# Kernel tuning notes

Hardware: AMD Instinct MI355X
Metric: run time of the kernel (lower is better)

## Reference

```python
import jax, jax.numpy as jnp
import numpy as np

E = 1024
H = 16
D = E // H  # projection_dim = 64


def setup_inputs() -> dict:
    key = jax.random.key(0)
    ks = jax.random.split(key, 9)
    s = 1.0 / np.sqrt(E)
    return {
        "inputs": jax.random.normal(ks[0], (2, 2048, E), dtype=jnp.float32),
        "Wq": jax.random.uniform(ks[1], (E, E), jnp.float32, -s, s),
        "bq": jax.random.uniform(ks[2], (E,), jnp.float32, -s, s),
        "Wk": jax.random.uniform(ks[3], (E, E), jnp.float32, -s, s),
        "bk": jax.random.uniform(ks[4], (E,), jnp.float32, -s, s),
        "Wv": jax.random.uniform(ks[5], (E, E), jnp.float32, -s, s),
        "bv": jax.random.uniform(ks[6], (E,), jnp.float32, -s, s),
        "Wo": jax.random.uniform(ks[7], (E, E), jnp.float32, -s, s),
        "bo": jax.random.uniform(ks[8], (E,), jnp.float32, -s, s),
    }


def reference(inputs, Wq, bq, Wk, bk, Wv, bv, Wo, bo):
    B, S, _ = inputs.shape
    # Linear layers use y = x @ W.T + b (torch convention); weights here stored as [E,E]
    q = inputs @ Wq.T + bq
    k = inputs @ Wk.T + bk
    v = inputs @ Wv.T + bv
    # separate heads: [B,S,E] -> [B,H,S,D]
    q = q.reshape(B, S, H, D).transpose(0, 2, 1, 3)
    k = k.reshape(B, S, H, D).transpose(0, 2, 1, 3)
    v = v.reshape(B, S, H, D).transpose(0, 2, 1, 3)
    scale = 1.0 / jnp.sqrt(jnp.float32(D))
    scores = jnp.einsum('bhqd,bhkd->bhqk', q, k) * scale  # [B,H,S,S]
    weights = jax.nn.softmax(scores, axis=-1)
    attn = jnp.einsum('bhqk,bhkd->bhqd', weights, v)  # [B,H,S,D]
    concat = attn.transpose(0, 2, 1, 3).reshape(B, S, E)
    # dropout is identity in eval mode
    return concat @ Wo.T + bo
```

## Files before the change

kernel.cpp:

```cpp
#include <hip/hip_runtime.h>
#include <hip/hip_bf16.h>
#include <stdint.h>

#define E_ 1024
#define H_ 16
#define D_ 64
#define B_ 2
#define S_ 2048
#define M_ 4096

typedef __bf16 bf16_t;
typedef __bf16 bf16x8 __attribute__((ext_vector_type(8)));
typedef __bf16 bf16x4 __attribute__((ext_vector_type(4)));
typedef __bf16 bf16x2 __attribute__((ext_vector_type(2)));
typedef float  f32x4  __attribute__((ext_vector_type(4)));
typedef float  f32x16 __attribute__((ext_vector_type(16)));
typedef unsigned int u32x2 __attribute__((ext_vector_type(2)));
typedef unsigned int u32x4 __attribute__((ext_vector_type(4)));

__global__ __launch_bounds__(256) void cvt_f32_to_bf16(const float* __restrict__ src,
                                                       bf16_t* __restrict__ dst, int n4) {
  int i = blockIdx.x * blockDim.x + threadIdx.x;
  if (i < n4) {
    float4 v = reinterpret_cast<const float4*>(src)[i];
    bf16x4 o;
    o[0] = (bf16_t)v.x; o[1] = (bf16_t)v.y; o[2] = (bf16_t)v.z; o[3] = (bf16_t)v.w;
    reinterpret_cast<bf16x4*>(dst)[i] = o;
  }
}

__global__ __launch_bounds__(256) void cvt_weights(
    const float* __restrict__ w0, const float* __restrict__ w1,
    const float* __restrict__ w2, const float* __restrict__ w3,
    bf16_t* __restrict__ d0, bf16_t* __restrict__ d1,
    bf16_t* __restrict__ d2, bf16_t* __restrict__ d3) {
  const int z = blockIdx.y;
  const float* src = (z == 0) ? w0 : (z == 1) ? w1 : (z == 2) ? w2 : w3;
  bf16_t* dst = (z == 0) ? d0 : (z == 1) ? d1 : (z == 2) ? d2 : d3;
  int i = blockIdx.x * blockDim.x + threadIdx.x;
  float4 v = reinterpret_cast<const float4*>(src)[i];
  bf16x4 o;
  o[0] = (bf16_t)v.x; o[1] = (bf16_t)v.y; o[2] = (bf16_t)v.z; o[3] = (bf16_t)v.w;
  reinterpret_cast<bf16x4*>(dst)[i] = o;
}

static __device__ __forceinline__ void gl_lds16(const bf16_t* g, bf16_t* l) {
  __builtin_amdgcn_global_load_lds((__attribute__((address_space(1))) void*)g,
                                   (__attribute__((address_space(3))) void*)l,
                                   16, 0, 0);
}

__global__ __launch_bounds__(512) void qkv_gemm256(
    const bf16_t* __restrict__ xbf, const bf16_t* __restrict__ Wqkv,
    const float* __restrict__ bq, const float* __restrict__ bk, const float* __restrict__ bv,
    bf16_t* __restrict__ Qo, bf16_t* __restrict__ Ko, bf16_t* __restrict__ Vt) {
  __shared__ alignas(16) bf16_t lA[4][256 * 32];
  __shared__ alignas(16) bf16_t lB[4][256 * 32];
  const int tid = threadIdx.x, lane = tid & 63, wave = tid >> 6;
  const int wr = wave >> 2, wc = wave & 3;
  const int lrow = lane & 15, lgrp = lane >> 4;
  const int m0 = blockIdx.x << 8, n0 = blockIdx.y << 8;

  const int srow = tid >> 2;
  const int scolg = (tid & 3) ^ ((srow >> 1) & 3);
  const char* sA0 = (const char*)xbf  + (size_t)(m0 + srow) * 2048 + scolg * 16;
  const char* sB0 = (const char*)Wqkv + (size_t)(n0 + srow) * 2048 + scolg * 16;

  auto STAGE = [&](int T) {
    const int buf = T & 3;
    const char* a = sA0 + T * 64;
    const char* b = sB0 + T * 64;
    gl_lds16((const bf16_t*)a,                        &lA[buf][tid * 8]);
    gl_lds16((const bf16_t*)(a + (size_t)128 * 2048), &lA[buf][4096 + tid * 8]);
    gl_lds16((const bf16_t*)b,                        &lB[buf][tid * 8]);
    gl_lds16((const bf16_t*)(b + (size_t)128 * 2048), &lB[buf][4096 + tid * 8]);
  };

  f32x4 acc[8][4];
  const f32x4 zero = {0.f, 0.f, 0.f, 0.f};
#pragma unroll
  for (int i = 0; i < 8; i++)
#pragma unroll
    for (int j = 0; j < 4; j++) acc[i][j] = zero;

  const int rswz = (lgrp ^ ((lrow >> 1) & 3)) * 16;
  const int rdA = (wr * 128 + lrow) * 64 + rswz;
  const int rdB = (wc * 64 + lrow) * 64 + rswz;

  auto KTILE = [&](int T) {
    const int buf = T & 3;
    const char* kA = (const char*)&lA[buf][0] + rdA;
    const char* kB = (const char*)&lB[buf][0] + rdB;
    bf16x8 fA[8], fB[4];
#pragma unroll
    for (int i = 0; i < 8; i++) fA[i] = *reinterpret_cast<const bf16x8*>(kA + i * 1024);
#pragma unroll
    for (int j = 0; j < 4; j++) fB[j] = *reinterpret_cast<const bf16x8*>(kB + j * 1024);
    __builtin_amdgcn_s_setprio(1);
#pragma unroll
    for (int i = 0; i < 8; i++)
#pragma unroll
      for (int j = 0; j < 4; j++)
        acc[i][j] = __builtin_amdgcn_mfma_f32_16x16x32_bf16(fA[i], fB[j], acc[i][j], 0, 0, 0);
    __builtin_amdgcn_s_setprio(0);
  };

  STAGE(0); STAGE(1); STAGE(2);
  asm volatile("s_waitcnt vmcnt(8)" ::: "memory");
  __builtin_amdgcn_s_barrier();
  __builtin_amdgcn_sched_barrier(0);

  for (int T = 0; T < 29; ++T) {
    STAGE(T + 3);
    KTILE(T);
    asm volatile("s_waitcnt vmcnt(8)" ::: "memory");
    __builtin_amdgcn_s_barrier();
    __builtin_amdgcn_sched_barrier(0);
  }
  KTILE(29);
  asm volatile("s_waitcnt vmcnt(4)" ::: "memory");
  __builtin_amdgcn_s_barrier();
  __builtin_amdgcn_sched_barrier(0);
  KTILE(30);
  asm volatile("s_waitcnt vmcnt(0)" ::: "memory");
  __builtin_amdgcn_s_barrier();
  __builtin_amdgcn_sched_barrier(0);
  KTILE(31);

  const int z = n0 >> 10;
  const float* bias = (z == 0) ? bq : ((z == 1) ? bk : bv);
  const int nloc_base = (n0 & 1023) + wc * 64;
  if (z == 2) {
#pragma unroll
    for (int i = 0; i < 8; i++) {
      const int mb = m0 + wr * 128 + i * 16 + lgrp * 4;
      const int b_ = mb >> 11, s = mb & (S_ - 1);
#pragma unroll
      for (int j = 0; j < 4; j++) {
        const int nl = nloc_base + j * 16 + lrow;
        const float bn = bias[nl];
        const int h = nl >> 6, d = nl & 63;
        bf16x4 v;
#pragma unroll
        for (int r = 0; r < 4; r++) v[r] = (bf16_t)(acc[i][j][r] + bn);
        *reinterpret_cast<bf16x4*>(Vt + ((size_t)((b_ * H_ + h) * D_ + d)) * S_ + s) = v;
      }
    }
  } else {
    bf16_t* O = z ? Ko : Qo;
    const float scale = (z == 0) ? 0.18033688011112042f : 1.0f;
#pragma unroll
    for (int i = 0; i < 8; i++) {
      const int mb = m0 + wr * 128 + i * 16 + lgrp * 4;
      const int b_ = mb >> 11, s = mb & (S_ - 1);
#pragma unroll
      for (int j = 0; j < 4; j++) {
        const int nl = nloc_base + j * 16 + lrow;
        const float bn = bias[nl];
        const int h = nl >> 6, d = nl & 63;
#pragma unroll
        for (int r = 0; r < 4; r++)
          O[((size_t)((b_ * H_ + h) * S_) + (s + r)) * D_ + d] = (bf16_t)((acc[i][j][r] + bn) * scale);
      }
    }
  }
}

template <int SWAP>
static __device__ __forceinline__ void gemm128_mainloop(
    const bf16_t* __restrict__ Ag, const bf16_t* __restrict__ Bg,
    bf16_t* ldsA0, bf16_t* ldsA1, bf16_t* ldsB0, bf16_t* ldsB1,
    int m0, int n0, f32x4 acc[4][4]) {
  const int tid  = threadIdx.x;
  const int lane = tid & 63, wave = tid >> 6;
  const int lrow = lane & 15, lgrp = lane >> 4;
  const int wr = (wave >> 1) * 64, wc = (wave & 1) * 64;
  const int skol = (lane & 3) * 8;
  const int c0 = wave * 2;
  const int rowA = c0 * 16 + (lane >> 2);
  const f32x4 zero = {0.f, 0.f, 0.f, 0.f};
#pragma unroll
  for (int i = 0; i < 4; i++)
#pragma unroll
    for (int j = 0; j < 4; j++) acc[i][j] = zero;

  gl_lds16(Ag + (size_t)(m0 + rowA) * E_ + skol,      ldsA0 + c0 * 512);
  gl_lds16(Ag + (size_t)(m0 + rowA + 16) * E_ + skol, ldsA0 + (c0 + 1) * 512);
  gl_lds16(Bg + (size_t)(n0 + rowA) * E_ + skol,      ldsB0 + c0 * 512);
  gl_lds16(Bg + (size_t)(n0 + rowA + 16) * E_ + skol, ldsB0 + (c0 + 1) * 512);
  __syncthreads();

  for (int kt = 0; kt < E_ / 32; ++kt) {
    bf16_t* sA = (kt & 1) ? ldsA1 : ldsA0;
    bf16_t* sB = (kt & 1) ? ldsB1 : ldsB0;
    if (kt + 1 < E_ / 32) {
      bf16_t* dA = (kt & 1) ? ldsA0 : ldsA1;
      bf16_t* dB = (kt & 1) ? ldsB0 : ldsB1;
      const int k0 = (kt + 1) * 32;
      gl_lds16(Ag + (size_t)(m0 + rowA) * E_ + k0 + skol,      dA + c0 * 512);
      gl_lds16(Ag + (size_t)(m0 + rowA + 16) * E_ + k0 + skol, dA + (c0 + 1) * 512);
      gl_lds16(Bg + (size_t)(n0 + rowA) * E_ + k0 + skol,      dB + c0 * 512);
      gl_lds16(Bg + (size_t)(n0 + rowA + 16) * E_ + k0 + skol, dB + (c0 + 1) * 512);
    }
    bf16x8 fA[4], fB[4];
#pragma unroll
    for (int i = 0; i < 4; i++)
      fA[i] = *reinterpret_cast<const bf16x8*>(sA + (wr + i * 16 + lrow) * 32 + lgrp * 8);
#pragma unroll
    for (int j = 0; j < 4; j++)
      fB[j] = *reinterpret_cast<const bf16x8*>(sB + (wc + j * 16 + lrow) * 32 + lgrp * 8);
#pragma unroll
    for (int i = 0; i < 4; i++)
#pragma unroll
      for (int j = 0; j < 4; j++)
        acc[i][j] = SWAP
          ? __builtin_amdgcn_mfma_f32_16x16x32_bf16(fB[j], fA[i], acc[i][j], 0, 0, 0)
          : __builtin_amdgcn_mfma_f32_16x16x32_bf16(fA[i], fB[j], acc[i][j], 0, 0, 0);
    __syncthreads();
  }
}

__global__ __launch_bounds__(256) void out_gemm(
    const bf16_t* __restrict__ Cbf, const bf16_t* __restrict__ Wob,
    const float* __restrict__ bo, float* __restrict__ out) {
  __shared__ alignas(16) bf16_t ldsA[2][128 * 32];
  __shared__ alignas(16) bf16_t ldsB[2][128 * 32];
  const int m0 = blockIdx.x * 128, n0 = blockIdx.y * 128;
  f32x4 acc[4][4];
  gemm128_mainloop<1>(Cbf, Wob, ldsA[0], ldsA[1], ldsB[0], ldsB[1], m0, n0, acc);

  const int lane = threadIdx.x & 63, wave = threadIdx.x >> 6;
  const int lrow = lane & 15, lgrp = lane >> 4;
  const int wr = (wave >> 1) * 64, wc = (wave & 1) * 64;
#pragma unroll
  for (int i = 0; i < 4; i++) {
    const int m = m0 + wr + i * 16 + lrow;
#pragma unroll
    for (int j = 0; j < 4; j++) {
      const int nb = n0 + wc + j * 16 + lgrp * 4;
      const f32x4 b4 = *reinterpret_cast<const f32x4*>(bo + nb);
      f32x4 v = acc[i][j] + b4;
      *reinterpret_cast<f32x4*>(out + (size_t)m * E_ + nb) = v;
    }
  }
}


static __device__ __forceinline__ unsigned pack2(float a, float b) {
  bf16x2 t; t[0] = (bf16_t)a; t[1] = (bf16_t)b;
  return __builtin_bit_cast(unsigned, t);
}

static __device__ __forceinline__ bf16x8 mkfrag(unsigned a0, unsigned a1,
                                                unsigned a2, unsigned a3) {
  u32x2 s02 = __builtin_amdgcn_permlane32_swap(a0, a2, false, false);
  u32x2 s13 = __builtin_amdgcn_permlane32_swap(a1, a3, false, false);
  u32x4 t; t[0] = s02[0]; t[1] = s13[0]; t[2] = s02[1]; t[3] = s13[1];
  return *reinterpret_cast<bf16x8*>(&t);
}

__global__ __launch_bounds__(512) void attn_kernel(
    const bf16_t* __restrict__ Qg, const bf16_t* __restrict__ Kg,
    const bf16_t* __restrict__ Vtg, bf16_t* __restrict__ Og) {
  __shared__ alignas(16) bf16_t Kl[2][2][64 * 64];
  __shared__ alignas(16) bf16_t Vl[2][2][64 * 64];
  const int f = blockIdx.x;
  const int bh = (f & 7) * 4 + (f >> 7);
  const int q0 = ((f >> 3) & 15) * 128;
  const int tid = threadIdx.x, lane = tid & 63, wave = tid >> 6;
  const int qsub = wave & 3, kvg = wave >> 2;
  const int ql = lane & 31, hi = lane >> 5;
  const bf16_t* Qb = Qg + (size_t)bh * S_ * D_;
  const bf16_t* Kb = Kg + (size_t)bh * S_ * D_;
  const bf16_t* Vb = Vtg + (size_t)bh * D_ * S_;

  const int q = q0 + qsub * 32 + ql;
  bf16x8 qf[4];
#pragma unroll
  for (int ds = 0; ds < 4; ds++)
    qf[ds] = *reinterpret_cast<const bf16x8*>(Qb + (size_t)q * D_ + ds * 16 + hi * 8);

  f32x16 o0, o1;
#pragma unroll
  for (int r = 0; r < 16; r++) { o0[r] = 0.f; o1[r] = 0.f; }
  float li = 0.f;

  const int srow_lo = lane >> 3;
  const int sunit = lane & 7;

#pragma unroll
  for (int p = 0; p < 2; p++) {
    int c = p * 4 + qsub;
    int row = c * 8 + srow_lo;
    int u = sunit ^ (row & 7);
    gl_lds16(Kb + (size_t)(kvg * 64 + row) * D_ + u * 8, &Kl[kvg][0][c * 512]);
    gl_lds16(Vb + (size_t)row * S_ + kvg * 64 + u * 8, &Vl[kvg][0][c * 512]);
  }
  __syncthreads();

  for (int it = 0; it < S_ / 128; ++it) {
    const int cur = it & 1;
    if (it + 1 < S_ / 128) {
      const int kvn = (kvg + (it + 1) * 2) * 64;
#pragma unroll
      for (int p = 0; p < 2; p++) {
        int c = p * 4 + qsub;
        int row = c * 8 + srow_lo;
        int u = sunit ^ (row & 7);
        gl_lds16(Kb + (size_t)(kvn + row) * D_ + u * 8, &Kl[kvg][cur ^ 1][c * 512]);
        gl_lds16(Vb + (size_t)row * S_ + kvn + u * 8, &Vl[kvg][cur ^ 1][c * 512]);
      }
    }
    const char* kbuf = reinterpret_cast<const char*>(&Kl[kvg][cur][0]);
    const char* vbuf = reinterpret_cast<const char*>(&Vl[kvg][cur][0]);

    f32x16 pa0, pa1;
#pragma unroll
    for (int r = 0; r < 16; r++) { pa0[r] = 0.f; pa1[r] = 0.f; }
    __builtin_amdgcn_s_setprio(1);
#pragma unroll
    for (int ds = 0; ds < 4; ds++) {
      {
        const int krow = ql;
        const int u = (ds * 2 + hi) ^ (krow & 7);
        bf16x8 kf = *reinterpret_cast<const bf16x8*>(kbuf + krow * 128 + u * 16);
        pa0 = __builtin_amdgcn_mfma_f32_32x32x16_bf16(kf, qf[ds], pa0, 0, 0, 0);
      }
      {
        const int krow = 32 + ql;
        const int u = (ds * 2 + hi) ^ (krow & 7);
        bf16x8 kf = *reinterpret_cast<const bf16x8*>(kbuf + krow * 128 + u * 16);
        pa1 = __builtin_amdgcn_mfma_f32_32x32x16_bf16(kf, qf[ds], pa1, 0, 0, 0);
      }
    }
    __builtin_amdgcn_s_setprio(0);

    float ps = 0.f;
#pragma unroll
    for (int r = 0; r < 16; r++) {
      pa0[r] = __builtin_amdgcn_exp2f(pa0[r]); ps += pa0[r];
      pa1[r] = __builtin_amdgcn_exp2f(pa1[r]); ps += pa1[r];
    }
    {
      u32x2 ss = __builtin_amdgcn_permlane32_swap(
          __builtin_bit_cast(unsigned, ps), __builtin_bit_cast(unsigned, ps), false, false);
      ps = __builtin_bit_cast(float, ss[0]) + __builtin_bit_cast(float, ss[1]);
    }
    li += ps;

    unsigned w0[8], w1[8];
#pragma unroll
    for (int i = 0; i < 8; i++) {
      w0[i] = pack2(pa0[2 * i], pa0[2 * i + 1]);
      w1[i] = pack2(pa1[2 * i], pa1[2 * i + 1]);
    }
    bf16x8 bfr[4];
    bfr[0] = mkfrag(w0[0], w0[1], w0[2], w0[3]);
    bfr[1] = mkfrag(w0[4], w0[5], w0[6], w0[7]);
    bfr[2] = mkfrag(w1[0], w1[1], w1[2], w1[3]);
    bfr[3] = mkfrag(w1[4], w1[5], w1[6], w1[7]);

    __builtin_amdgcn_s_setprio(1);
#pragma unroll
    for (int step = 0; step < 4; step++) {
      {
        const int vrow = ql;
        const int u = (step * 2 + hi) ^ (vrow & 7);
        bf16x8 vf = *reinterpret_cast<const bf16x8*>(vbuf + vrow * 128 + u * 16);
        o0 = __builtin_amdgcn_mfma_f32_32x32x16_bf16(vf, bfr[step], o0, 0, 0, 0);
      }
      {
        const int vrow = 32 + ql;
        const int u = (step * 2 + hi) ^ (vrow & 7);
        bf16x8 vf = *reinterpret_cast<const bf16x8*>(vbuf + vrow * 128 + u * 16);
        o1 = __builtin_amdgcn_mfma_f32_32x32x16_bf16(vf, bfr[step], o1, 0, 0, 0);
      }
    }
    __builtin_amdgcn_s_setprio(0);

    __syncthreads();
  }

  f32x4* smO = reinterpret_cast<f32x4*>(&Kl[0][0][0]);
  float* smL = reinterpret_cast<float*>(&Vl[0][0][0]);
  const int mi_ = qsub * 64 + lane;
  if (kvg == 1) {
#pragma unroll
    for (int g = 0; g < 4; g++) {
      f32x4 a;
#pragma unroll
      for (int i = 0; i < 4; i++) a[i] = o0[g * 4 + i];
      smO[g * 256 + mi_] = a;
    }
#pragma unroll
    for (int g = 0; g < 4; g++) {
      f32x4 a;
#pragma unroll
      for (int i = 0; i < 4; i++) a[i] = o1[g * 4 + i];
      smO[(g + 4) * 256 + mi_] = a;
    }
    smL[mi_] = li;
  }
  __syncthreads();
  if (kvg == 0) {
    li += smL[mi_];
#pragma unroll
    for (int g = 0; g < 4; g++) {
      f32x4 a = smO[g * 256 + mi_];
#pragma unroll
      for (int i = 0; i < 4; i++) o0[g * 4 + i] += a[i];
    }
#pragma unroll
    for (int g = 0; g < 4; g++) {
      f32x4 a = smO[(g + 4) * 256 + mi_];
#pragma unroll
      for (int i = 0; i < 4; i++) o1[g * 4 + i] += a[i];
    }
    const float inv = 1.0f / li;
    const int b = bh >> 4, h = bh & 15;
    bf16_t* orow = Og + (size_t)(b * S_ + q) * E_ + h * 64;
#pragma unroll
    for (int g = 0; g < 4; g++) {
      bf16x4 v;
#pragma unroll
      for (int i = 0; i < 4; i++) v[i] = (bf16_t)(o0[g * 4 + i] * inv);
      *reinterpret_cast<bf16x4*>(orow + g * 8 + hi * 4) = v;
    }
#pragma unroll
    for (int g = 0; g < 4; g++) {
      bf16x4 v;
#pragma unroll
      for (int i = 0; i < 4; i++) v[i] = (bf16_t)(o1[g * 4 + i] * inv);
      *reinterpret_cast<bf16x4*>(orow + 32 + g * 8 + hi * 4) = v;
    }
  }
}

extern "C" void kernel_launch(void* const* d_in, const int* in_sizes, int n_in,
                              void* d_out, int out_size, void* d_ws, size_t ws_size,
                              hipStream_t stream) {
  (void)in_sizes; (void)n_in; (void)out_size; (void)ws_size;
  const float* x  = (const float*)d_in[0];
  const float* Wq = (const float*)d_in[1];
  const float* bq = (const float*)d_in[2];
  const float* Wk = (const float*)d_in[3];
  const float* bk = (const float*)d_in[4];
  const float* Wv = (const float*)d_in[5];
  const float* bv = (const float*)d_in[6];
  const float* Wo = (const float*)d_in[7];
  const float* bo = (const float*)d_in[8];
  float* out = (float*)d_out;

  bf16_t* ws  = (bf16_t*)d_ws;
  bf16_t* xbf = ws;
  bf16_t* Ct  = ws;
  bf16_t* wqb = ws + (4u << 20);
  bf16_t* wkb = ws + (5u << 20);
  bf16_t* wvb = ws + (6u << 20);
  bf16_t* wob = ws + (7u << 20);
  bf16_t* Qt  = ws + (8u << 20);
  bf16_t* Kt  = ws + (12u << 20);
  bf16_t* Vt  = ws + (16u << 20);

  cvt_f32_to_bf16<<<4096, 256, 0, stream>>>(x, xbf, 1 << 20);
  cvt_weights<<<dim3(1024, 4), 256, 0, stream>>>(Wq, Wk, Wv, Wo, wqb, wkb, wvb, wob);

  qkv_gemm256<<<dim3(16, 12), 512, 0, stream>>>(xbf, wqb, bq, bk, bv, Qt, Kt, Vt);
  attn_kernel<<<512, 512, 0, stream>>>(Qt, Kt, Vt, Ct);
  out_gemm<<<dim3(32, 8), 256, 0, stream>>>(Ct, wob, bo, out);
}
```

Before: 124.4 us.

## Restructure QKV GEMM into double-buffered K=64 tiles with phased ping-pong schedule

Replaces the 4-stage K=32 LDS pipeline of the QKV projection GEMM with 2 LDS buffers of K=64 tiles and an 8-wide XOR swizzle. Each tile is split into four sub-phases over half-M and half-N quadrants. Global-to-LDS loads for the next buffer are spread across those phases, with explicit vmcnt/lgkmcnt waits and barriers around each MFMA burst. The aim is finer interleaving of loads, LDS reads and MFMAs and fewer pipeline bubbles. The cost is more barriers per K step and less prefetch depth.

```diff
diff --git a/kernel.cpp b/kernel.cpp
--- a/kernel.cpp
+++ b/kernel.cpp
@@ -54,27 +54,31 @@
     const bf16_t* __restrict__ xbf, const bf16_t* __restrict__ Wqkv,
     const float* __restrict__ bq, const float* __restrict__ bk, const float* __restrict__ bv,
     bf16_t* __restrict__ Qo, bf16_t* __restrict__ Ko, bf16_t* __restrict__ Vt) {
-  __shared__ alignas(16) bf16_t lA[4][256 * 32];
-  __shared__ alignas(16) bf16_t lB[4][256 * 32];
+  __shared__ alignas(16) bf16_t lA[2][256 * 64];
+  __shared__ alignas(16) bf16_t lB[2][256 * 64];
   const int tid = threadIdx.x, lane = tid & 63, wave = tid >> 6;
   const int wr = wave >> 2, wc = wave & 3;
   const int lrow = lane & 15, lgrp = lane >> 4;
   const int m0 = blockIdx.x << 8, n0 = blockIdx.y << 8;
 
-  const int srow = tid >> 2;
-  const int scolg = (tid & 3) ^ ((srow >> 1) & 3);
-  const char* sA0 = (const char*)xbf  + (size_t)(m0 + srow) * 2048 + scolg * 16;
-  const char* sB0 = (const char*)Wqkv + (size_t)(n0 + srow) * 2048 + scolg * 16;
-
-  auto STAGE = [&](int T) {
-    const int buf = T & 3;
-    const char* a = sA0 + T * 64;
-    const char* b = sB0 + T * 64;
-    gl_lds16((const bf16_t*)a,                        &lA[buf][tid * 8]);
-    gl_lds16((const bf16_t*)(a + (size_t)128 * 2048), &lA[buf][4096 + tid * 8]);
-    gl_lds16((const bf16_t*)b,                        &lB[buf][tid * 8]);
-    gl_lds16((const bf16_t*)(b + (size_t)128 * 2048), &lB[buf][4096 + tid * 8]);
-  };
+  const int srow = tid >> 3, sslot = tid & 7;
+
+#define STAGE_A(ND, RBASE, KT) do {                                              \
+    _Pragma("unroll") for (int l_ = 0; l_ < 2; ++l_) {                           \
+      const int rl_ = l_ * 64 + srow;                                            \
+      const char* s_ = (const char*)xbf + (size_t)(m0 + (RBASE) + rl_) * 2048    \
+                       + (KT) * 128 + ((sslot ^ (rl_ & 7)) << 4);                \
+      gl_lds16((const bf16_t*)s_, &lA[ND][(RBASE) * 64 + l_ * 4096 + tid * 8]);  \
+    }                                                                            \
+  } while (0)
+#define STAGE_B(ND, RBASE, KT) do {                                              \
+    _Pragma("unroll") for (int l_ = 0; l_ < 2; ++l_) {                           \
+      const int rl_ = l_ * 64 + srow;                                            \
+      const char* s_ = (const char*)Wqkv + (size_t)(n0 + (RBASE) + rl_) * 2048   \
+                       + (KT) * 128 + ((sslot ^ (rl_ & 7)) << 4);                \
+      gl_lds16((const bf16_t*)s_, &lB[ND][(RBASE) * 64 + l_ * 4096 + tid * 8]);  \
+    }                                                                            \
+  } while (0)
 
   f32x4 acc[8][4];
   const f32x4 zero = {0.f, 0.f, 0.f, 0.f};
@@ -83,49 +87,58 @@
 #pragma unroll
     for (int j = 0; j < 4; j++) acc[i][j] = zero;
 
-  const int rswz = (lgrp ^ ((lrow >> 1) & 3)) * 16;
-  const int rdA = (wr * 128 + lrow) * 64 + rswz;
-  const int rdB = (wc * 64 + lrow) * 64 + rswz;
-
-  auto KTILE = [&](int T) {
-    const int buf = T & 3;
-    const char* kA = (const char*)&lA[buf][0] + rdA;
-    const char* kB = (const char*)&lB[buf][0] + rdB;
-    bf16x8 fA[8], fB[4];
-#pragma unroll
-    for (int i = 0; i < 8; i++) fA[i] = *reinterpret_cast<const bf16x8*>(kA + i * 1024);
-#pragma unroll
-    for (int j = 0; j < 4; j++) fB[j] = *reinterpret_cast<const bf16x8*>(kB + j * 1024);
-    __builtin_amdgcn_s_setprio(1);
-#pragma unroll
-    for (int i = 0; i < 8; i++)
-#pragma unroll
-      for (int j = 0; j < 4; j++)
-        acc[i][j] = __builtin_amdgcn_mfma_f32_16x16x32_bf16(fA[i], fB[j], acc[i][j], 0, 0, 0);
-    __builtin_amdgcn_s_setprio(0);
-  };
-
-  STAGE(0); STAGE(1); STAGE(2);
-  asm volatile("s_waitcnt vmcnt(8)" ::: "memory");
+#define PHASE(D, MH, NH, VM, STAGE_STMT) do {                                    \
+    bf16x8 fA_[2][4], fB_[2][2];                                                 \
+    const char* Ab_ = (const char*)&lA[D][0];                                    \
+    const char* Bb_ = (const char*)&lB[D][0];                                    \
+    _Pragma("unroll") for (int ks_ = 0; ks_ < 2; ks_++) {                        \
+      _Pragma("unroll") for (int i_ = 0; i_ < 4; i_++) {                         \
+        const int row_ = wr * 128 + (MH) * 64 + i_ * 16 + lrow;                  \
+        const int sl_ = (ks_ * 4 + lgrp) ^ (lrow & 7);                           \
+        fA_[ks_][i_] = *reinterpret_cast<const bf16x8*>(Ab_ + row_ * 128 + sl_ * 16); \
+      }                                                                          \
+      _Pragma("unroll") for (int j_ = 0; j_ < 2; j_++) {                         \
+        const int row_ = wc * 64 + (NH) * 32 + j_ * 16 + lrow;                   \
+        const int sl_ = (ks_ * 4 + lgrp) ^ (lrow & 7);                           \
+        fB_[ks_][j_] = *reinterpret_cast<const bf16x8*>(Bb_ + row_ * 128 + sl_ * 16); \
+      }                                                                          \
+    }                                                                            \
+    STAGE_STMT;                                                                  \
+    asm volatile("s_waitcnt lgkmcnt(8)" ::: "memory");                           \
+    asm volatile("s_waitcnt vmcnt(" #VM ")" ::: "memory");                       \
+    __builtin_amdgcn_sched_barrier(0);                                           \
+    __builtin_amdgcn_s_barrier();                                                \
+    asm volatile("s_waitcnt lgkmcnt(0)" ::: "memory");                           \
+    __builtin_amdgcn_sched_barrier(0);                                           \
+    __builtin_amdgcn_s_setprio(1);                                               \
+    _Pragma("unroll") for (int i_ = 0; i_ < 4; i_++)                             \
+      _Pragma("unroll") for (int j_ = 0; j_ < 2; j_++)                           \
+        _Pragma("unroll") for (int ks_ = 0; ks_ < 2; ks_++)                      \
+          acc[(MH) * 4 + i_][(NH) * 2 + j_] = __builtin_amdgcn_mfma_f32_16x16x32_bf16( \
+              fA_[ks_][i_], fB_[ks_][j_], acc[(MH) * 4 + i_][(NH) * 2 + j_], 0, 0, 0); \
+    __builtin_amdgcn_s_setprio(0);                                               \
+    __builtin_amdgcn_s_barrier();                                                \
+  } while (0)
+
+  STAGE_A(0, 0, 0); STAGE_B(0, 0, 0); STAGE_A(0, 128, 0); STAGE_B(0, 128, 0);
+  asm volatile("s_waitcnt vmcnt(0)" ::: "memory");
+  __builtin_amdgcn_sched_barrier(0);
   __builtin_amdgcn_s_barrier();
-  __builtin_amdgcn_sched_barrier(0);
-
-  for (int T = 0; T < 29; ++T) {
-    STAGE(T + 3);
-    KTILE(T);
-    asm volatile("s_waitcnt vmcnt(8)" ::: "memory");
-    __builtin_amdgcn_s_barrier();
-    __builtin_amdgcn_sched_barrier(0);
-  }
-  KTILE(29);
-  asm volatile("s_waitcnt vmcnt(4)" ::: "memory");
-  __builtin_amdgcn_s_barrier();
-  __builtin_amdgcn_sched_barrier(0);
-  KTILE(30);
-  asm volatile("s_waitcnt vmcnt(0)" ::: "memory");
-  __builtin_amdgcn_s_barrier();
-  __builtin_amdgcn_sched_barrier(0);
-  KTILE(31);
+
+  for (int t = 0; t < 8; ++t) {
+    const int k1 = 2 * t + 1;
+    PHASE(0, 0, 0, 8, { STAGE_A(1, 0, k1);   STAGE_B(1, 0, k1); });
+    PHASE(0, 0, 1, 8, { STAGE_A(1, 128, k1); STAGE_B(1, 128, k1); });
+    PHASE(0, 1, 0, 4, );
+    PHASE(0, 1, 1, 0, );
+    PHASE(1, 0, 0, 8, if (t < 7) { STAGE_A(0, 0, k1 + 1);   STAGE_B(0, 0, k1 + 1); });
+    PHASE(1, 0, 1, 8, if (t < 7) { STAGE_A(0, 128, k1 + 1); STAGE_B(0, 128, k1 + 1); });
+    PHASE(1, 1, 0, 4, );
+    PHASE(1, 1, 1, 0, );
+  }
+#undef PHASE
+#undef STAGE_A
+#undef STAGE_B
 
   const int z = n0 >> 10;
   const float* bias = (z == 0) ? bq : ((z == 1) ? bk : bv);
```

Result: no change. 123.4 us (-0.8%).
